# Kernel tuning notes

Measured on AMD Instinct MI355X. Metric: run time of the kernel, lower is better.

Reference implementation:

```python
import jax, jax.numpy as jnp
import numpy as np

MEL_W = 1.0
GATE_W = 1.0
ATT_W = 0.1
GA_W = 0.1
SIGMA = 0.4


def setup_inputs() -> dict:
    key = jax.random.key(0)
    ks = jax.random.split(key, 8)
    B, M, T_OUT, T_IN = 64, 80, 2000, 400
    mel_out = jax.random.normal(ks[0], (B, M, T_OUT), dtype=jnp.float32)
    mel_out_postnet = jax.random.normal(ks[1], (B, M, T_OUT), dtype=jnp.float32)
    gate_out = jax.random.normal(ks[2], (B, T_OUT), dtype=jnp.float32)
    align = jax.random.uniform(ks[3], (B, T_OUT, T_IN), dtype=jnp.float32)
    alignments = align / jnp.sum(align, axis=-1, keepdims=True)  # attention-like rows
    mel_target = jax.random.normal(ks[4], (B, M, T_OUT), dtype=jnp.float32)
    gate_target = jax.random.uniform(ks[5], (B, T_OUT), dtype=jnp.float32)
    input_lengths = jax.random.randint(ks[6], (B,), T_IN // 2, T_IN + 1, dtype=jnp.int32)
    output_lengths = jax.random.randint(ks[7], (B,), T_OUT // 2, T_OUT + 1, dtype=jnp.int32)
    return {
        "mel_out": mel_out,
        "mel_out_postnet": mel_out_postnet,
        "gate_out": gate_out,
        "alignments": alignments,
        "mel_target": mel_target,
        "gate_target": gate_target,
        "input_lengths": input_lengths,
        "output_lengths": output_lengths,
    }


def _bce_with_logits(logits, targets):
    # mean of: max(x,0) - x*z + log(1 + exp(-|x|))  (numerically stable)
    return jnp.mean(jnp.maximum(logits, 0.0) - logits * targets
                    + jnp.log1p(jnp.exp(-jnp.abs(logits))))


def reference(mel_out, mel_out_postnet, gate_out, alignments,
              mel_target, gate_target, input_lengths, output_lengths):
    B, T_out, T_in = alignments.shape

    # Mel L1 loss (decoder + postnet)
    mel_loss = (jnp.mean(jnp.abs(mel_out - mel_target))
                + jnp.mean(jnp.abs(mel_out_postnet - mel_target)))

    # Gate BCE-with-logits
    gate_loss = _bce_with_logits(gate_out, gate_target)

    # Monotonic attention penalty: sum of attention strictly below the diagonal
    ii = jnp.arange(T_out)[:, None]   # [T_out, 1]
    jj = jnp.arange(T_in)[None, :]    # [1, T_in]
    backward_mask = (jj < ii).astype(alignments.dtype)  # 1 - triu(ones, 0)
    att_loss = jnp.sum(alignments * backward_mask[None]) / B

    # Guided attention: Gaussian anti-diagonal mask, zero outside valid lengths
    T_in_b = input_lengths.astype(jnp.float32)[:, None, None]    # [B,1,1]
    T_out_b = output_lengths.astype(jnp.float32)[:, None, None]  # [B,1,1]
    i_f = jnp.arange(T_out, dtype=jnp.float32)[None, :, None]    # [1,T_out,1]
    j_f = jnp.arange(T_in, dtype=jnp.float32)[None, None, :]     # [1,1,T_in]
    expected_j = j_f / T_in_b * T_out_b
    w = 1.0 - jnp.exp(-(i_f - expected_j) ** 2 / (2.0 * SIGMA ** 2))
    valid = (jnp.arange(T_out)[None, :, None] < output_lengths[:, None, None]) & \
            (jnp.arange(T_in)[None, None, :] < input_lengths[:, None, None])
    guided = jnp.where(valid, w, 0.0)  # [B, T_out, T_in]
    ga_loss = jnp.sum(alignments * guided) / B

    total = (MEL_W * mel_loss + GATE_W * gate_loss
             + ATT_W * att_loss + GA_W * ga_loss)
    return (total, mel_loss, gate_loss, att_loss, ga_loss)
```

## Files before the change

### kernel.cpp

```cpp
#include <hip/hip_runtime.h>
#include <math.h>

constexpr int Bsz   = 64;
constexpr int Mmel  = 80;
constexpr int Tout  = 2000;
constexpr int Tin   = 400;
constexpr int MEL_N  = Bsz * Mmel * Tout;
constexpr int GATE_N = Bsz * Tout;
constexpr int ALN_N  = Bsz * Tout * Tin;
constexpr int TIN4   = Tin / 4;

constexpr float ATT_W = 0.1f;
constexpr float GA_W  = 0.1f;
constexpr float INV_2SIG2 = 3.125f;

constexpr int NBLK = 6144;
constexpr int NTHR = 256;

__device__ __forceinline__ float wave_reduce(float v) {
    #pragma unroll
    for (int off = 32; off > 0; off >>= 1)
        v += __shfl_down(v, off, 64);
    return v;
}

__device__ __forceinline__ double wave_reduce_d(double v) {
    #pragma unroll
    for (int off = 32; off > 0; off >>= 1)
        v += __shfl_down(v, off, 64);
    return v;
}

__device__ __forceinline__ void process_aln(
    float4 a, int i,
    const int* __restrict__ s_il, const int* __restrict__ s_ol,
    const float* __restrict__ s_scale,
    float& att_s, float& ga_s)
{
    const int row  = i / TIN4;
    const int j0   = (i - row * TIN4) * 4;
    const int irow = row % Tout;
    const int b    = row / Tout;
    const int il   = s_il[b];
    const int ol   = s_ol[b];
    const float scale = s_scale[b];
    const bool row_valid = irow < ol;
    const float fi = (float)irow;

    const float av[4] = {a.x, a.y, a.z, a.w};
    #pragma unroll
    for (int k = 0; k < 4; ++k) {
        const int jj = j0 + k;
        att_s += (jj < irow) ? av[k] : 0.0f;
        const float d = fi - (float)jj * scale;
        const float w = 1.0f - __expf(-d * d * INV_2SIG2);
        ga_s += (row_valid && jj < il) ? av[k] * w : 0.0f;
    }
}

__global__ __launch_bounds__(NTHR) void loss_main(
    const float* __restrict__ mel_out,
    const float* __restrict__ mel_post,
    const float* __restrict__ gate_out,
    const float* __restrict__ align,
    const float* __restrict__ mel_tgt,
    const float* __restrict__ gate_tgt,
    const int*   __restrict__ in_len,
    const int*   __restrict__ out_len,
    float4* __restrict__ partials)
{
    __shared__ int   s_il[Bsz];
    __shared__ int   s_ol[Bsz];
    __shared__ float s_scale[Bsz];
    if (threadIdx.x < Bsz) {
        const int il = in_len[threadIdx.x];
        const int ol = out_len[threadIdx.x];
        s_il[threadIdx.x] = il;
        s_ol[threadIdx.x] = ol;
        s_scale[threadIdx.x] = (float)ol / (float)il;
    }
    __syncthreads();

    const int tid    = blockIdx.x * blockDim.x + threadIdx.x;
    const int stride = gridDim.x * blockDim.x;

    float mel_s = 0.f, gate_s = 0.f, att_s = 0.f, ga_s = 0.f;

    {
        const float4* a4 = (const float4*)mel_out;
        const float4* p4 = (const float4*)mel_post;
        const float4* t4 = (const float4*)mel_tgt;
        const int n4 = MEL_N / 4;
        int i = tid;
        for (; i + stride < n4; i += 2 * stride) {
            const int i1 = i + stride;
            float4 a0 = a4[i],  a1 = a4[i1];
            float4 p0 = p4[i],  p1 = p4[i1];
            float4 t0 = t4[i],  t1 = t4[i1];
            mel_s += fabsf(a0.x - t0.x) + fabsf(a0.y - t0.y) + fabsf(a0.z - t0.z) + fabsf(a0.w - t0.w);
            mel_s += fabsf(p0.x - t0.x) + fabsf(p0.y - t0.y) + fabsf(p0.z - t0.z) + fabsf(p0.w - t0.w);
            mel_s += fabsf(a1.x - t1.x) + fabsf(a1.y - t1.y) + fabsf(a1.z - t1.z) + fabsf(a1.w - t1.w);
            mel_s += fabsf(p1.x - t1.x) + fabsf(p1.y - t1.y) + fabsf(p1.z - t1.z) + fabsf(p1.w - t1.w);
        }
        for (; i < n4; i += stride) {
            float4 a = a4[i], p = p4[i], t = t4[i];
            mel_s += fabsf(a.x - t.x) + fabsf(a.y - t.y) + fabsf(a.z - t.z) + fabsf(a.w - t.w);
            mel_s += fabsf(p.x - t.x) + fabsf(p.y - t.y) + fabsf(p.z - t.z) + fabsf(p.w - t.w);
        }
    }

    {
        const float4* x4 = (const float4*)gate_out;
        const float4* z4 = (const float4*)gate_tgt;
        const int n4 = GATE_N / 4;
        for (int i = tid; i < n4; i += stride) {
            float4 x = x4[i], z = z4[i];
            gate_s += fmaxf(x.x, 0.f) - x.x * z.x + log1pf(expf(-fabsf(x.x)));
            gate_s += fmaxf(x.y, 0.f) - x.y * z.y + log1pf(expf(-fabsf(x.y)));
            gate_s += fmaxf(x.z, 0.f) - x.z * z.z + log1pf(expf(-fabsf(x.z)));
            gate_s += fmaxf(x.w, 0.f) - x.w * z.w + log1pf(expf(-fabsf(x.w)));
        }
    }

    {
        const float4* al4 = (const float4*)align;
        const int n4 = ALN_N / 4;
        int i = tid;
        for (; i + 3 * stride < n4; i += 4 * stride) {
            float4 a0 = al4[i];
            float4 a1 = al4[i + stride];
            float4 a2 = al4[i + 2 * stride];
            float4 a3 = al4[i + 3 * stride];
            process_aln(a0, i,              s_il, s_ol, s_scale, att_s, ga_s);
            process_aln(a1, i + stride,     s_il, s_ol, s_scale, att_s, ga_s);
            process_aln(a2, i + 2 * stride, s_il, s_ol, s_scale, att_s, ga_s);
            process_aln(a3, i + 3 * stride, s_il, s_ol, s_scale, att_s, ga_s);
        }
        for (; i < n4; i += stride)
            process_aln(al4[i], i, s_il, s_ol, s_scale, att_s, ga_s);
    }

    __shared__ float smem[NTHR / 64][4];
    const int lane = threadIdx.x & 63;
    const int wid  = threadIdx.x >> 6;

    mel_s  = wave_reduce(mel_s);
    gate_s = wave_reduce(gate_s);
    att_s  = wave_reduce(att_s);
    ga_s   = wave_reduce(ga_s);
    if (lane == 0) {
        smem[wid][0] = mel_s;
        smem[wid][1] = gate_s;
        smem[wid][2] = att_s;
        smem[wid][3] = ga_s;
    }
    __syncthreads();
    if (threadIdx.x == 0) {
        float m = 0.f, g = 0.f, at = 0.f, ga = 0.f;
        #pragma unroll
        for (int w = 0; w < NTHR / 64; ++w) {
            m  += smem[w][0];
            g  += smem[w][1];
            at += smem[w][2];
            ga += smem[w][3];
        }
        partials[blockIdx.x] = make_float4(m, g, at, ga);
    }
}

__global__ __launch_bounds__(512) void loss_final(
    const float4* __restrict__ partials, float* __restrict__ out)
{
    double m = 0.0, g = 0.0, at = 0.0, ga = 0.0;
    for (int i = threadIdx.x; i < NBLK; i += 512) {
        float4 p = partials[i];
        m += p.x; g += p.y; at += p.z; ga += p.w;
    }
    m  = wave_reduce_d(m);
    g  = wave_reduce_d(g);
    at = wave_reduce_d(at);
    ga = wave_reduce_d(ga);

    __shared__ double smem[8][4];
    const int lane = threadIdx.x & 63;
    const int wid  = threadIdx.x >> 6;
    if (lane == 0) {
        smem[wid][0] = m; smem[wid][1] = g; smem[wid][2] = at; smem[wid][3] = ga;
    }
    __syncthreads();
    if (threadIdx.x == 0) {
        double ms = 0, gs = 0, ats = 0, gas = 0;
        #pragma unroll
        for (int w = 0; w < 8; ++w) {
            ms += smem[w][0]; gs += smem[w][1]; ats += smem[w][2]; gas += smem[w][3];
        }
        const double mel  = ms  / (double)MEL_N;
        const double gate = gs  / (double)GATE_N;
        const double att  = ats / (double)Bsz;
        const double gav  = gas / (double)Bsz;
        const double total = mel + gate + (double)ATT_W * att + (double)GA_W * gav;
        out[0] = (float)total;
        out[1] = (float)mel;
        out[2] = (float)gate;
        out[3] = (float)att;
        out[4] = (float)gav;
    }
}

extern "C" void kernel_launch(void* const* d_in, const int* in_sizes, int n_in,
                              void* d_out, int out_size, void* d_ws, size_t ws_size,
                              hipStream_t stream) {
    const float* mel_out  = (const float*)d_in[0];
    const float* mel_post = (const float*)d_in[1];
    const float* gate_out = (const float*)d_in[2];
    const float* align    = (const float*)d_in[3];
    const float* mel_tgt  = (const float*)d_in[4];
    const float* gate_tgt = (const float*)d_in[5];
    const int*   in_len   = (const int*)d_in[6];
    const int*   out_len  = (const int*)d_in[7];

    float4* partials = (float4*)d_ws;

    loss_main<<<NBLK, NTHR, 0, stream>>>(mel_out, mel_post, gate_out, align,
                                         mel_tgt, gate_tgt, in_len, out_len, partials);
    loss_final<<<1, 512, 0, stream>>>(partials, (float*)d_out);
}
```

Measured before the change: 372.7 us.

## Map alignment rows to waves and cut per-element index math

```diff
diff --git a/kernel.cpp b/kernel.cpp
--- a/kernel.cpp
+++ b/kernel.cpp
@@ -7,15 +7,16 @@
 constexpr int Tin   = 400;
 constexpr int MEL_N  = Bsz * Mmel * Tout;
 constexpr int GATE_N = Bsz * Tout;
-constexpr int ALN_N  = Bsz * Tout * Tin;
+constexpr int ROWS   = Bsz * Tout;
 constexpr int TIN4   = Tin / 4;
 
 constexpr float ATT_W = 0.1f;
 constexpr float GA_W  = 0.1f;
-constexpr float INV_2SIG2 = 3.125f;
-
-constexpr int NBLK = 6144;
-constexpr int NTHR = 256;
+constexpr float NEG_C = -3.125f * 1.44269504088896340736f;
+
+constexpr int NBLK   = 2048;
+constexpr int NTHR   = 256;
+constexpr int NWAVES = NBLK * NTHR / 64;
 
 __device__ __forceinline__ float wave_reduce(float v) {
     #pragma unroll
@@ -31,30 +32,20 @@
     return v;
 }
 
-__device__ __forceinline__ void process_aln(
-    float4 a, int i,
-    const int* __restrict__ s_il, const int* __restrict__ s_ol,
-    const float* __restrict__ s_scale,
-    float& att_s, float& ga_s)
+__device__ __forceinline__ void proc4(float4 a, float jb, float fi,
+                                      float ilf, float olf, float sc,
+                                      float& att_s, float& ga_s)
 {
-    const int row  = i / TIN4;
-    const int j0   = (i - row * TIN4) * 4;
-    const int irow = row % Tout;
-    const int b    = row / Tout;
-    const int il   = s_il[b];
-    const int ol   = s_ol[b];
-    const float scale = s_scale[b];
-    const bool row_valid = irow < ol;
-    const float fi = (float)irow;
-
+    const bool rv = fi < olf;
     const float av[4] = {a.x, a.y, a.z, a.w};
     #pragma unroll
     for (int k = 0; k < 4; ++k) {
-        const int jj = j0 + k;
-        att_s += (jj < irow) ? av[k] : 0.0f;
-        const float d = fi - (float)jj * scale;
-        const float w = 1.0f - __expf(-d * d * INV_2SIG2);
-        ga_s += (row_valid && jj < il) ? av[k] * w : 0.0f;
+        const float jf = jb + (float)k;
+        att_s += (jf < fi) ? av[k] : 0.0f;
+        const float d = fmaf(-jf, sc, fi);
+        const float e = exp2f(d * d * NEG_C);
+        const float g = av[k] - av[k] * e;
+        ga_s += (rv && (jf < ilf)) ? g : 0.0f;
     }
 }
 
@@ -69,15 +60,15 @@
     const int*   __restrict__ out_len,
     float4* __restrict__ partials)
 {
-    __shared__ int   s_il[Bsz];
-    __shared__ int   s_ol[Bsz];
-    __shared__ float s_scale[Bsz];
+    __shared__ float s_ilf[Bsz];
+    __shared__ float s_olf[Bsz];
+    __shared__ float s_sc[Bsz];
     if (threadIdx.x < Bsz) {
-        const int il = in_len[threadIdx.x];
-        const int ol = out_len[threadIdx.x];
-        s_il[threadIdx.x] = il;
-        s_ol[threadIdx.x] = ol;
-        s_scale[threadIdx.x] = (float)ol / (float)il;
+        const float il = (float)in_len[threadIdx.x];
+        const float ol = (float)out_len[threadIdx.x];
+        s_ilf[threadIdx.x] = il;
+        s_olf[threadIdx.x] = ol;
+        s_sc[threadIdx.x]  = ol / il;
     }
     __syncthreads();
 
@@ -124,20 +115,48 @@
 
     {
         const float4* al4 = (const float4*)align;
-        const int n4 = ALN_N / 4;
-        int i = tid;
-        for (; i + 3 * stride < n4; i += 4 * stride) {
-            float4 a0 = al4[i];
-            float4 a1 = al4[i + stride];
-            float4 a2 = al4[i + 2 * stride];
-            float4 a3 = al4[i + 3 * stride];
-            process_aln(a0, i,              s_il, s_ol, s_scale, att_s, ga_s);
-            process_aln(a1, i + stride,     s_il, s_ol, s_scale, att_s, ga_s);
-            process_aln(a2, i + 2 * stride, s_il, s_ol, s_scale, att_s, ga_s);
-            process_aln(a3, i + 3 * stride, s_il, s_ol, s_scale, att_s, ga_s);
-        }
-        for (; i < n4; i += stride)
-            process_aln(al4[i], i, s_il, s_ol, s_scale, att_s, ga_s);
+        const int wv   = (blockIdx.x << 2) | (threadIdx.x >> 6);
+        const int lane = threadIdx.x & 63;
+        const float jb0 = (float)(4 * lane);
+        const float jb1 = jb0 + 256.0f;
+        const bool tail = lane < (TIN4 - 64);
+
+        int r = wv;
+        for (; r + NWAVES < ROWS; r += 2 * NWAVES) {
+            const int r1 = r + NWAVES;
+            const int b0 = r  / Tout;
+            const int b1 = r1 / Tout;
+            const int ir0 = r  - b0 * Tout;
+            const int ir1 = r1 - b1 * Tout;
+            const float4* rp0 = al4 + (size_t)r  * TIN4;
+            const float4* rp1 = al4 + (size_t)r1 * TIN4;
+            float4 a00 = rp0[lane];
+            float4 a10 = rp1[lane];
+            float4 a01 = make_float4(0.f, 0.f, 0.f, 0.f);
+            float4 a11 = make_float4(0.f, 0.f, 0.f, 0.f);
+            if (tail) a01 = rp0[lane + 64];
+            if (tail) a11 = rp1[lane + 64];
+
+            const float fi0 = (float)ir0, fi1 = (float)ir1;
+            const float il0 = s_ilf[b0], ol0 = s_olf[b0], sc0 = s_sc[b0];
+            const float il1 = s_ilf[b1], ol1 = s_olf[b1], sc1 = s_sc[b1];
+
+            proc4(a00, jb0, fi0, il0, ol0, sc0, att_s, ga_s);
+            proc4(a01, jb1, fi0, il0, ol0, sc0, att_s, ga_s);
+            proc4(a10, jb0, fi1, il1, ol1, sc1, att_s, ga_s);
+            proc4(a11, jb1, fi1, il1, ol1, sc1, att_s, ga_s);
+        }
+        for (; r < ROWS; r += NWAVES) {
+            const int b  = r / Tout;
+            const int ir = r - b * Tout;
+            const float4* rp = al4 + (size_t)r * TIN4;
+            float4 a0 = rp[lane];
+            float4 a1 = make_float4(0.f, 0.f, 0.f, 0.f);
+            if (tail) a1 = rp[lane + 64];
+            const float fi = (float)ir;
+            proc4(a0, jb0, fi, s_ilf[b], s_olf[b], s_sc[b], att_s, ga_s);
+            proc4(a1, jb1, fi, s_ilf[b], s_olf[b], s_sc[b], att_s, ga_s);
+        }
     }
 
     __shared__ float smem[NTHR / 64][4];
```

Result: no change. 377.6 us (+1.3%).
